# Kernel optimization log

Measured on AMD Instinct MI355X. Metric: run time of the kernel, lower is better.

Reference implementation:

```python
import jax, jax.numpy as jnp
import numpy as np

ALPHA = 0.2  # LeakyReLU negative slope
NEG_BIG = -9e15


def setup_inputs() -> dict:
    key = jax.random.key(0)
    k1, k2, k3, k4 = jax.random.split(key, 4)
    N, F_IN, F_OUT = 8192, 256, 128
    h = jax.random.normal(k1, (N, F_IN), dtype=jnp.float32)
    adj = jax.random.randint(k2, (N, N), 0, 2, dtype=jnp.int32)
    # xavier_uniform with gain=1.414
    def xavier(k, shape, gain=1.414):
        fan_in, fan_out = shape[0], shape[1]
        bound = gain * np.sqrt(6.0 / (fan_in + fan_out))
        return jax.random.uniform(k, shape, jnp.float32, -bound, bound)
    W = xavier(k3, (F_IN, F_OUT))
    a = xavier(k4, (2 * F_OUT, 1))
    return {"h": h, "adj": adj, "W": W, "a": a}


def reference(h, adj, W, a):
    # Wh: [N, F_out]
    Wh = h @ W
    F_out = W.shape[1]
    a1 = a[:F_out, 0]   # attends to source (row) node
    a2 = a[F_out:, 0]   # attends to target (col) node
    # Additive decomposition of concat([Wh_i, Wh_j]) @ a:
    # e[i, j] = leaky_relu(Wh_i . a1 + Wh_j . a2)
    f1 = Wh @ a1  # [N]
    f2 = Wh @ a2  # [N]
    e = jax.nn.leaky_relu(f1[:, None] + f2[None, :], negative_slope=ALPHA)  # [N, N]
    scores = jnp.where(adj > 0, e, jnp.float32(NEG_BIG))
    attention = jax.nn.softmax(scores, axis=1)
    # dropout is identity in eval mode (training=False)
    h_prime = attention @ Wh  # [N, F_out]
    return h_prime
```

## Files before the change

kernel.cpp:

```cpp
#include <hip/hip_runtime.h>


#define N_NODES 8192
#define F_IN 256
#define F_OUT 128
#define RPB 32
#define JCH 128
#define JSPLIT 4
#define JRANGE (N_NODES / JSPLIT)
#define NCH (JRANGE / JCH)

typedef _Float16 half8 __attribute__((ext_vector_type(8)));
typedef float floatx4 __attribute__((ext_vector_type(4)));
typedef float f32x4 __attribute__((ext_vector_type(4)));
typedef int intx4 __attribute__((ext_vector_type(4)));

__device__ __align__(16) float g_Wh[N_NODES * F_OUT];
__device__ __align__(16) _Float16 g_WhT[(size_t)F_OUT * N_NODES];
__device__ __align__(16) float g_f1[N_NODES];
__device__ __align__(16) float g_f2[N_NODES];
__device__ __align__(16) float g_part[JSPLIT][N_NODES * F_OUT];
__device__ __align__(16) float g_spart[JSPLIT][N_NODES];
__device__ __align__(16) unsigned char g_bits[(size_t)N_NODES * (N_NODES / 8)];

__global__ __launch_bounds__(256, 2) void prep_kernel(
    const int* __restrict__ adj, const float* __restrict__ h,
    const float* __restrict__ W, const float* __restrict__ a) {
  const int t = threadIdx.x;
  const int bid = blockIdx.x;

  if (bid < N_NODES / 8) {
    const int wave = t >> 6;
    const int lane = t & 63;
    const int row0 = bid * 8 + wave * 2;
#pragma unroll 1
    for (int rr = 0; rr < 2; ++rr) {
      const int r = row0 + rr;
      const int* rowp = adj + (size_t)r * N_NODES;
#pragma unroll 4
      for (int p = 0; p < 16; ++p) {
        const int j0 = p * 512 + lane * 8;
        const intx4 v0 = __builtin_nontemporal_load((const intx4*)(rowp + j0));
        const intx4 v1 = __builtin_nontemporal_load((const intx4*)(rowp + j0 + 4));
        unsigned int byte = 0;
        byte |= (v0.x != 0) ? 1u : 0u;
        byte |= (v0.y != 0) ? 2u : 0u;
        byte |= (v0.z != 0) ? 4u : 0u;
        byte |= (v0.w != 0) ? 8u : 0u;
        byte |= (v1.x != 0) ? 16u : 0u;
        byte |= (v1.y != 0) ? 32u : 0u;
        byte |= (v1.z != 0) ? 64u : 0u;
        byte |= (v1.w != 0) ? 128u : 0u;
        const int b = p * 64 + lane;
        const int addr = r * 1024 + (((b >> 2) & 3) * 4 + (b & 3)) * 64 + (b >> 4);
        g_bits[addr] = (unsigned char)byte;
      }
    }
    return;
  }

  __shared__ float hT[F_IN][20];
  __shared__ float fs[2][2][8][2];
  const int i0 = (bid - N_NODES / 8) * 16;
  {
    const int row = t >> 4;
    const int fu = t & 15;
#pragma unroll
    for (int r = 0; r < 4; ++r) {
      const int ku = r * 16 + fu;
      const f32x4 v = __builtin_nontemporal_load(
          (const f32x4*)(h + (size_t)(i0 + row) * F_IN + ku * 4));
      hT[ku * 4 + 0][row] = v.x; hT[ku * 4 + 1][row] = v.y;
      hT[ku * 4 + 2][row] = v.z; hT[ku * 4 + 3][row] = v.w;
    }
  }
  __syncthreads();
  const int c = t & 127;
  const int rg = t >> 7;
  float acc[8];
#pragma unroll
  for (int r = 0; r < 8; ++r) acc[r] = 0.f;
#pragma unroll 8
  for (int k = 0; k < F_IN; ++k) {
    const float wv = W[k * F_OUT + c];
    const float4 x0 = *(const float4*)(&hT[k][rg * 8]);
    const float4 x1 = *(const float4*)(&hT[k][rg * 8 + 4]);
    acc[0] = fmaf(x0.x, wv, acc[0]); acc[1] = fmaf(x0.y, wv, acc[1]);
    acc[2] = fmaf(x0.z, wv, acc[2]); acc[3] = fmaf(x0.w, wv, acc[3]);
    acc[4] = fmaf(x1.x, wv, acc[4]); acc[5] = fmaf(x1.y, wv, acc[5]);
    acc[6] = fmaf(x1.z, wv, acc[6]); acc[7] = fmaf(x1.w, wv, acc[7]);
  }
#pragma unroll
  for (int r = 0; r < 8; ++r)
    g_Wh[(size_t)(i0 + rg * 8 + r) * F_OUT + c] = acc[r];
  union { _Float16 hh[8]; uint4 u4; } pk;
#pragma unroll
  for (int r = 0; r < 8; ++r) pk.hh[r] = (_Float16)acc[r];
  *(uint4*)(g_WhT + (size_t)c * N_NODES + i0 + rg * 8) = pk.u4;

  const float a1c = a[c];
  const float a2c = a[F_OUT + c];
  float p1[8], p2[8];
#pragma unroll
  for (int r = 0; r < 8; ++r) { p1[r] = acc[r] * a1c; p2[r] = acc[r] * a2c; }
#pragma unroll
  for (int o = 32; o > 0; o >>= 1)
#pragma unroll
    for (int r = 0; r < 8; ++r) {
      p1[r] += __shfl_down(p1[r], o, 64);
      p2[r] += __shfl_down(p2[r], o, 64);
    }
  const int wv = t >> 6;
  const int lane = t & 63;
  if (lane == 0) {
#pragma unroll
    for (int r = 0; r < 8; ++r) {
      fs[wv >> 1][wv & 1][r][0] = p1[r];
      fs[wv >> 1][wv & 1][r][1] = p2[r];
    }
  }
  __syncthreads();
  if (t < 16) {
    const int rg2 = t >> 3, r2 = t & 7;
    g_f1[i0 + rg2 * 8 + r2] = fs[rg2][0][r2][0] + fs[rg2][1][r2][0];
    g_f2[i0 + rg2 * 8 + r2] = fs[rg2][0][r2][1] + fs[rg2][1][r2][1];
  }
}

__device__ __forceinline__ float score_b(unsigned int bit, float f2v, float f1r) {
  float s = f1r + f2v;
  s = fmaxf(s, 0.2f * s);
  float arg = bit ? fmaf(s, 1.44269504088896f, -16.0f) : -1.0e5f;
  return __builtin_amdgcn_exp2f(arg);
}

__global__ __launch_bounds__(256, 2) void gat_attn_kernel() {
  const int t = threadIdx.x;
  const int wave = t >> 6;
  const int lane = t & 63;
  const int mrow = lane & 15;
  const int quad = lane >> 4;
  const int flat = blockIdx.x;
  const int js = flat & 3;
  const int i0 = (flat >> 2) * RPB;
  const int jbase = js * JRANGE;

  __shared__ float ldsF2[JRANGE];
  __shared__ float ldsO[RPB][F_OUT];
  __shared__ float ldsS[4][RPB];

  int rm[4], cm[4];
  {
    half8 a1f, b1f, a2f, b2f;
#pragma unroll
    for (int e = 0; e < 8; ++e) {
      a1f[e] = (_Float16)0; b1f[e] = (_Float16)0;
      a2f[e] = (_Float16)0; b2f[e] = (_Float16)0;
    }
    if (quad == 0) {
      a1f[0] = (_Float16)mrow; b1f[0] = (_Float16)1;
      a2f[0] = (_Float16)1;    b2f[0] = (_Float16)mrow;
    }
    floatx4 d1 = (floatx4)0.f, d2 = (floatx4)0.f;
    d1 = __builtin_amdgcn_mfma_f32_16x16x32_f16(a1f, b1f, d1, 0, 0, 0);
    d2 = __builtin_amdgcn_mfma_f32_16x16x32_f16(a2f, b2f, d2, 0, 0, 0);
#pragma unroll
    for (int r = 0; r < 4; ++r) { rm[r] = (int)d1[r]; cm[r] = (int)d2[r]; }
  }

  const float f1r0 = g_f1[i0 + mrow];
  const float f1r1 = g_f1[i0 + 16 + mrow];

  half8 ones;
#pragma unroll
  for (int e = 0; e < 8; ++e) ones[e] = (_Float16)1;

  floatx4 acc[2][8];
  floatx4 asum[2];
#pragma unroll
  for (int tl = 0; tl < 2; ++tl) {
    asum[tl] = (floatx4)0.f;
#pragma unroll
    for (int ct = 0; ct < 8; ++ct) acc[tl][ct] = (floatx4)0.f;
  }

#pragma unroll
  for (int it = 0; it < 2; ++it) {
    const int u = it * 256 + t;
    *(float4*)&ldsF2[u * 4] = *(const float4*)(g_f2 + jbase + u * 4);
  }
  __syncthreads();

  const int wq = wave * 4 + quad;
  const int jloc = wave * 32 + quad * 8;
  const unsigned char* bp0 = g_bits + (i0 + mrow) * 1024 + wq * 64 + js * (JRANGE / 128);
  const unsigned char* bp1 = g_bits + (i0 + 16 + mrow) * 1024 + wq * 64 + js * (JRANGE / 128);

#pragma unroll 1
  for (int c4 = 0; c4 < NCH / 4; ++c4) {
    const unsigned int dw0 =
        __builtin_nontemporal_load((const unsigned int*)(bp0 + c4 * 4));
    const unsigned int dw1 =
        __builtin_nontemporal_load((const unsigned int*)(bp1 + c4 * 4));
#pragma unroll
    for (int k = 0; k < 4; ++k) {
      const int c = c4 * 4 + k;
      const int jglob = jbase + c * JCH + jloc;

      half8 bfr[8];
#pragma unroll
      for (int ct = 0; ct < 8; ++ct)
        bfr[ct] = *(const half8*)(g_WhT + (size_t)(ct * 16 + mrow) * N_NODES + jglob);

      const float4 F0 = *(const float4*)&ldsF2[c * JCH + jloc];
      const float4 F1 = *(const float4*)&ldsF2[c * JCH + jloc + 4];

      const unsigned int b0 = (dw0 >> (8 * k)) & 0xffu;
      const unsigned int b1 = (dw1 >> (8 * k)) & 0xffu;

      half8 af0, af1;
      af0[0] = (_Float16)score_b(b0 & 1u,   F0.x, f1r0);
      af0[1] = (_Float16)score_b(b0 & 2u,   F0.y, f1r0);
      af0[2] = (_Float16)score_b(b0 & 4u,   F0.z, f1r0);
      af0[3] = (_Float16)score_b(b0 & 8u,   F0.w, f1r0);
      af0[4] = (_Float16)score_b(b0 & 16u,  F1.x, f1r0);
      af0[5] = (_Float16)score_b(b0 & 32u,  F1.y, f1r0);
      af0[6] = (_Float16)score_b(b0 & 64u,  F1.z, f1r0);
      af0[7] = (_Float16)score_b(b0 & 128u, F1.w, f1r0);
      af1[0] = (_Float16)score_b(b1 & 1u,   F0.x, f1r1);
      af1[1] = (_Float16)score_b(b1 & 2u,   F0.y, f1r1);
      af1[2] = (_Float16)score_b(b1 & 4u,   F0.z, f1r1);
      af1[3] = (_Float16)score_b(b1 & 8u,   F0.w, f1r1);
      af1[4] = (_Float16)score_b(b1 & 16u,  F1.x, f1r1);
      af1[5] = (_Float16)score_b(b1 & 32u,  F1.y, f1r1);
      af1[6] = (_Float16)score_b(b1 & 64u,  F1.z, f1r1);
      af1[7] = (_Float16)score_b(b1 & 128u, F1.w, f1r1);

#pragma unroll
      for (int ct = 0; ct < 8; ++ct) {
        acc[0][ct] = __builtin_amdgcn_mfma_f32_16x16x32_f16(af0, bfr[ct], acc[0][ct], 0, 0, 0);
        acc[1][ct] = __builtin_amdgcn_mfma_f32_16x16x32_f16(af1, bfr[ct], acc[1][ct], 0, 0, 0);
      }
      asum[0] = __builtin_amdgcn_mfma_f32_16x16x32_f16(af0, ones, asum[0], 0, 0, 0);
      asum[1] = __builtin_amdgcn_mfma_f32_16x16x32_f16(af1, ones, asum[1], 0, 0, 0);
    }
  }

  if (mrow == 0) {
#pragma unroll
    for (int tl = 0; tl < 2; ++tl)
#pragma unroll
      for (int r = 0; r < 4; ++r)
        ldsS[wave][tl * 16 + rm[r]] = asum[tl][r];
  }
  for (int w = 0; w < 4; ++w) {
    if (wave == w) {
#pragma unroll
      for (int tl = 0; tl < 2; ++tl)
#pragma unroll
        for (int ct = 0; ct < 8; ++ct)
#pragma unroll
          for (int r = 0; r < 4; ++r) {
            float* p = &ldsO[tl * 16 + rm[r]][ct * 16 + cm[r]];
            if (w == 0) *p = acc[tl][ct][r];
            else        *p += acc[tl][ct][r];
          }
    }
    __syncthreads();
  }
  {
    const int row = t >> 3;
    const int c0 = (t & 7) * 16;
    float* dst = g_part[js] + (size_t)(i0 + row) * F_OUT + c0;
#pragma unroll
    for (int q = 0; q < 4; ++q)
      __builtin_nontemporal_store(*(const f32x4*)(&ldsO[row][c0 + q * 4]),
                                  (f32x4*)(dst + q * 4));
    if (t < RPB)
      g_spart[js][i0 + t] = ldsS[0][t] + ldsS[1][t] + ldsS[2][t] + ldsS[3][t];
  }
}

__global__ __launch_bounds__(256) void comb_kernel(float* __restrict__ out) {
  const int u = blockIdx.x * 256 + threadIdx.x;
  const int row = u >> 5;
  const float s = g_spart[0][row] + g_spart[1][row] +
                  g_spart[2][row] + g_spart[3][row];
  const f32x4 v = __builtin_nontemporal_load(((const f32x4*)g_part[0]) + u) +
                  __builtin_nontemporal_load(((const f32x4*)g_part[1]) + u) +
                  __builtin_nontemporal_load(((const f32x4*)g_part[2]) + u) +
                  __builtin_nontemporal_load(((const f32x4*)g_part[3]) + u);
  __builtin_nontemporal_store(v * (1.0f / s), ((f32x4*)out) + u);
}

extern "C" void kernel_launch(void* const* d_in, const int* in_sizes, int n_in,
                              void* d_out, int out_size, void* d_ws, size_t ws_size,
                              hipStream_t stream) {
  const float* h = (const float*)d_in[0];
  const int* adj = (const int*)d_in[1];
  const float* W = (const float*)d_in[2];
  const float* a = (const float*)d_in[3];
  float* out = (float*)d_out;
  (void)d_ws; (void)ws_size;

  prep_kernel<<<dim3(N_NODES / 8 + N_NODES / 16), dim3(256), 0, stream>>>(adj, h, W, a);
  gat_attn_kernel<<<dim3((N_NODES / RPB) * JSPLIT), dim3(256), 0, stream>>>();
  comb_kernel<<<dim3(N_NODES * F_OUT / 4 / 256), dim3(256), 0, stream>>>(out);
}
```

Measured before the change: 470.3 us.

## Stage WhT j-tiles in LDS and split attention over 32 column tiles

The attention kernel now gives each block a 256-column j-tile and 256 rows (8 waves). The fp16 WhT tile is staged once in padded shared memory, so the B operands are read from LDS instead of being re-gathered from global memory in every iteration. The adjacency bitmask is repacked so each lane reads its 8 bytes of mask in one load. The prep kernel interleaves bit-packing blocks with matmul blocks and no longer writes the unused fp32 Wh. In exchange, partial outputs grow from 4 to 32 slices, which adds a large amount of global write and read traffic in the combine kernel.

```diff
diff --git a/kernel.cpp b/kernel.cpp
--- a/kernel.cpp
+++ b/kernel.cpp
@@ -4,23 +4,21 @@
 #define N_NODES 8192
 #define F_IN 256
 #define F_OUT 128
-#define RPB 32
-#define JCH 128
-#define JSPLIT 4
-#define JRANGE (N_NODES / JSPLIT)
-#define NCH (JRANGE / JCH)
+#define NJT 32
+#define JTW 256
+#define NCH 8
+#define LDS_STRIDE 264
 
 typedef _Float16 half8 __attribute__((ext_vector_type(8)));
 typedef float floatx4 __attribute__((ext_vector_type(4)));
 typedef float f32x4 __attribute__((ext_vector_type(4)));
 typedef int intx4 __attribute__((ext_vector_type(4)));
 
-__device__ __align__(16) float g_Wh[N_NODES * F_OUT];
 __device__ __align__(16) _Float16 g_WhT[(size_t)F_OUT * N_NODES];
 __device__ __align__(16) float g_f1[N_NODES];
 __device__ __align__(16) float g_f2[N_NODES];
-__device__ __align__(16) float g_part[JSPLIT][N_NODES * F_OUT];
-__device__ __align__(16) float g_spart[JSPLIT][N_NODES];
+__device__ __align__(16) float g_part[NJT][N_NODES * F_OUT];
+__device__ __align__(16) float g_spart[NJT][N_NODES];
 __device__ __align__(16) unsigned char g_bits[(size_t)N_NODES * (N_NODES / 8)];
 
 __global__ __launch_bounds__(256, 2) void prep_kernel(
@@ -29,10 +27,11 @@
   const int t = threadIdx.x;
   const int bid = blockIdx.x;
 
-  if (bid < N_NODES / 8) {
+  if (bid % 3 != 0) {
+    const int pid = bid - (bid + 2) / 3;
     const int wave = t >> 6;
     const int lane = t & 63;
-    const int row0 = bid * 8 + wave * 2;
+    const int row0 = pid * 8 + wave * 2;
 #pragma unroll 1
     for (int rr = 0; rr < 2; ++rr) {
       const int r = row0 + rr;
@@ -52,8 +51,7 @@
         byte |= (v1.z != 0) ? 64u : 0u;
         byte |= (v1.w != 0) ? 128u : 0u;
         const int b = p * 64 + lane;
-        const int addr = r * 1024 + (((b >> 2) & 3) * 4 + (b & 3)) * 64 + (b >> 4);
-        g_bits[addr] = (unsigned char)byte;
+        g_bits[(size_t)r * 1024 + (b & 3) * 256 + (b >> 2)] = (unsigned char)byte;
       }
     }
     return;
@@ -61,7 +59,7 @@
 
   __shared__ float hT[F_IN][20];
   __shared__ float fs[2][2][8][2];
-  const int i0 = (bid - N_NODES / 8) * 16;
+  const int i0 = (bid / 3) * 16;
   {
     const int row = t >> 4;
     const int fu = t & 15;
@@ -90,9 +88,6 @@
     acc[4] = fmaf(x1.x, wv, acc[4]); acc[5] = fmaf(x1.y, wv, acc[5]);
     acc[6] = fmaf(x1.z, wv, acc[6]); acc[7] = fmaf(x1.w, wv, acc[7]);
   }
-#pragma unroll
-  for (int r = 0; r < 8; ++r)
-    g_Wh[(size_t)(i0 + rg * 8 + r) * F_OUT + c] = acc[r];
   union { _Float16 hh[8]; uint4 u4; } pk;
 #pragma unroll
   for (int r = 0; r < 8; ++r) pk.hh[r] = (_Float16)acc[r];
@@ -134,20 +129,25 @@
   return __builtin_amdgcn_exp2f(arg);
 }
 
-__global__ __launch_bounds__(256, 2) void gat_attn_kernel() {
+__global__ __launch_bounds__(512, 2) void gat_attn_kernel() {
   const int t = threadIdx.x;
   const int wave = t >> 6;
   const int lane = t & 63;
   const int mrow = lane & 15;
   const int quad = lane >> 4;
-  const int flat = blockIdx.x;
-  const int js = flat & 3;
-  const int i0 = (flat >> 2) * RPB;
-  const int jbase = js * JRANGE;
-
-  __shared__ float ldsF2[JRANGE];
-  __shared__ float ldsO[RPB][F_OUT];
-  __shared__ float ldsS[4][RPB];
+  const int bid = blockIdx.x;
+  const int jt = bid >> 5;
+  const int ig = bid & 31;
+  const int rowb = ig * 256 + wave * 32;
+
+  __shared__ _Float16 ldsWhT[F_OUT * LDS_STRIDE];
+  __shared__ float ldsF2[JTW];
+
+  const int r0 = rowb + mrow, r1 = rowb + 16 + mrow;
+  const uint2 AB0 = *(const uint2*)(g_bits + (size_t)r0 * 1024 + quad * 256 + jt * 8);
+  const uint2 AB1 = *(const uint2*)(g_bits + (size_t)r1 * 1024 + quad * 256 + jt * 8);
+  const float f1r0 = g_f1[r0];
+  const float f1r1 = g_f1[r1];
 
   int rm[4], cm[4];
   {
@@ -168,8 +168,15 @@
     for (int r = 0; r < 4; ++r) { rm[r] = (int)d1[r]; cm[r] = (int)d2[r]; }
   }
 
-  const float f1r0 = g_f1[i0 + mrow];
-  const float f1r1 = g_f1[i0 + 16 + mrow];
+#pragma unroll
+  for (int it = 0; it < 8; ++it) {
+    const int idx = it * 512 + t;
+    const int row = idx >> 5, cu = idx & 31;
+    *(half8*)&ldsWhT[row * LDS_STRIDE + cu * 8] =
+        *(const half8*)(g_WhT + (size_t)row * N_NODES + jt * JTW + cu * 8);
+  }
+  if (t < 64) *(float4*)&ldsF2[t * 4] = *(const float4*)(g_f2 + jt * JTW + t * 4);
+  __syncthreads();
 
   half8 ones;
 #pragma unroll
@@ -185,111 +192,75 @@
   }
 
 #pragma unroll
-  for (int it = 0; it < 2; ++it) {
-    const int u = it * 256 + t;
-    *(float4*)&ldsF2[u * 4] = *(const float4*)(g_f2 + jbase + u * 4);
-  }
-  __syncthreads();
-
-  const int wq = wave * 4 + quad;
-  const int jloc = wave * 32 + quad * 8;
-  const unsigned char* bp0 = g_bits + (i0 + mrow) * 1024 + wq * 64 + js * (JRANGE / 128);
-  const unsigned char* bp1 = g_bits + (i0 + 16 + mrow) * 1024 + wq * 64 + js * (JRANGE / 128);
-
-#pragma unroll 1
-  for (int c4 = 0; c4 < NCH / 4; ++c4) {
-    const unsigned int dw0 =
-        __builtin_nontemporal_load((const unsigned int*)(bp0 + c4 * 4));
-    const unsigned int dw1 =
-        __builtin_nontemporal_load((const unsigned int*)(bp1 + c4 * 4));
-#pragma unroll
-    for (int k = 0; k < 4; ++k) {
-      const int c = c4 * 4 + k;
-      const int jglob = jbase + c * JCH + jloc;
-
-      half8 bfr[8];
-#pragma unroll
-      for (int ct = 0; ct < 8; ++ct)
-        bfr[ct] = *(const half8*)(g_WhT + (size_t)(ct * 16 + mrow) * N_NODES + jglob);
-
-      const float4 F0 = *(const float4*)&ldsF2[c * JCH + jloc];
-      const float4 F1 = *(const float4*)&ldsF2[c * JCH + jloc + 4];
-
-      const unsigned int b0 = (dw0 >> (8 * k)) & 0xffu;
-      const unsigned int b1 = (dw1 >> (8 * k)) & 0xffu;
-
-      half8 af0, af1;
-      af0[0] = (_Float16)score_b(b0 & 1u,   F0.x, f1r0);
-      af0[1] = (_Float16)score_b(b0 & 2u,   F0.y, f1r0);
-      af0[2] = (_Float16)score_b(b0 & 4u,   F0.z, f1r0);
-      af0[3] = (_Float16)score_b(b0 & 8u,   F0.w, f1r0);
-      af0[4] = (_Float16)score_b(b0 & 16u,  F1.x, f1r0);
-      af0[5] = (_Float16)score_b(b0 & 32u,  F1.y, f1r0);
-      af0[6] = (_Float16)score_b(b0 & 64u,  F1.z, f1r0);
-      af0[7] = (_Float16)score_b(b0 & 128u, F1.w, f1r0);
-      af1[0] = (_Float16)score_b(b1 & 1u,   F0.x, f1r1);
-      af1[1] = (_Float16)score_b(b1 & 2u,   F0.y, f1r1);
-      af1[2] = (_Float16)score_b(b1 & 4u,   F0.z, f1r1);
-      af1[3] = (_Float16)score_b(b1 & 8u,   F0.w, f1r1);
-      af1[4] = (_Float16)score_b(b1 & 16u,  F1.x, f1r1);
-      af1[5] = (_Float16)score_b(b1 & 32u,  F1.y, f1r1);
-      af1[6] = (_Float16)score_b(b1 & 64u,  F1.z, f1r1);
-      af1[7] = (_Float16)score_b(b1 & 128u, F1.w, f1r1);
-
-#pragma unroll
-      for (int ct = 0; ct < 8; ++ct) {
-        acc[0][ct] = __builtin_amdgcn_mfma_f32_16x16x32_f16(af0, bfr[ct], acc[0][ct], 0, 0, 0);
-        acc[1][ct] = __builtin_amdgcn_mfma_f32_16x16x32_f16(af1, bfr[ct], acc[1][ct], 0, 0, 0);
-      }
-      asum[0] = __builtin_amdgcn_mfma_f32_16x16x32_f16(af0, ones, asum[0], 0, 0, 0);
-      asum[1] = __builtin_amdgcn_mfma_f32_16x16x32_f16(af1, ones, asum[1], 0, 0, 0);
-    }
-  }
-
+  for (int ch = 0; ch < NCH; ++ch) {
+    const int kb = ch * 32 + quad * 8;
+
+    half8 bfr[8];
+#pragma unroll
+    for (int ct = 0; ct < 8; ++ct)
+      bfr[ct] = *(const half8*)&ldsWhT[(ct * 16 + mrow) * LDS_STRIDE + kb];
+
+    const float4 F0 = *(const float4*)&ldsF2[kb];
+    const float4 F1 = *(const float4*)&ldsF2[kb + 4];
+
+    const unsigned int b0 = ((ch & 4) ? AB0.y : AB0.x) >> ((ch & 3) * 8);
+    const unsigned int b1 = ((ch & 4) ? AB1.y : AB1.x) >> ((ch & 3) * 8);
+
+    half8 af0, af1;
+    af0[0] = (_Float16)score_b(b0 & 1u,   F0.x, f1r0);
+    af0[1] = (_Float16)score_b(b0 & 2u,   F0.y, f1r0);
+    af0[2] = (_Float16)score_b(b0 & 4u,   F0.z, f1r0);
+    af0[3] = (_Float16)score_b(b0 & 8u,   F0.w, f1r0);
+    af0[4] = (_Float16)score_b(b0 & 16u,  F1.x, f1r0);
+    af0[5] = (_Float16)score_b(b0 & 32u,  F1.y, f1r0);
+    af0[6] = (_Float16)score_b(b0 & 64u,  F1.z, f1r0);
+    af0[7] = (_Float16)score_b(b0 & 128u, F1.w, f1r0);
+    af1[0] = (_Float16)score_b(b1 & 1u,   F0.x, f1r1);
+    af1[1] = (_Float16)score_b(b1 & 2u,   F0.y, f1r1);
+    af1[2] = (_Float16)score_b(b1 & 4u,   F0.z, f1r1);
+    af1[3] = (_Float16)score_b(b1 & 8u,   F0.w, f1r1);
+    af1[4] = (_Float16)score_b(b1 & 16u,  F1.x, f1r1);
+    af1[5] = (_Float16)score_b(b1 & 32u,  F1.y, f1r1);
+    af1[6] = (_Float16)score_b(b1 & 64u,  F1.z, f1r1);
+    af1[7] = (_Float16)score_b(b1 & 128u, F1.w, f1r1);
+
+#pragma unroll
+    for (int ct = 0; ct < 8; ++ct) {
+      acc[0][ct] = __builtin_amdgcn_mfma_f32_16x16x32_f16(af0, bfr[ct], acc[0][ct], 0, 0, 0);
+      acc[1][ct] = __builtin_amdgcn_mfma_f32_16x16x32_f16(af1, bfr[ct], acc[1][ct], 0, 0, 0);
+    }
+    asum[0] = __builtin_amdgcn_mfma_f32_16x16x32_f16(af0, ones, asum[0], 0, 0, 0);
+    asum[1] = __builtin_amdgcn_mfma_f32_16x16x32_f16(af1, ones, asum[1], 0, 0, 0);
+  }
+
+  float* pslice = g_part[jt];
+#pragma unroll
+  for (int tl = 0; tl < 2; ++tl)
+#pragma unroll
+    for (int ct = 0; ct < 8; ++ct)
+#pragma unroll
+      for (int r = 0; r < 4; ++r)
+        pslice[(size_t)(rowb + tl * 16 + rm[r]) * F_OUT + ct * 16 + cm[r]] =
+            acc[tl][ct][r];
   if (mrow == 0) {
 #pragma unroll
     for (int tl = 0; tl < 2; ++tl)
 #pragma unroll
       for (int r = 0; r < 4; ++r)
-        ldsS[wave][tl * 16 + rm[r]] = asum[tl][r];
-  }
-  for (int w = 0; w < 4; ++w) {
-    if (wave == w) {
-#pragma unroll
-      for (int tl = 0; tl < 2; ++tl)
-#pragma unroll
-        for (int ct = 0; ct < 8; ++ct)
-#pragma unroll
-          for (int r = 0; r < 4; ++r) {
-            float* p = &ldsO[tl * 16 + rm[r]][ct * 16 + cm[r]];
-            if (w == 0) *p = acc[tl][ct][r];
-            else        *p += acc[tl][ct][r];
-          }
-    }
-    __syncthreads();
-  }
-  {
-    const int row = t >> 3;
-    const int c0 = (t & 7) * 16;
-    float* dst = g_part[js] + (size_t)(i0 + row) * F_OUT + c0;
-#pragma unroll
-    for (int q = 0; q < 4; ++q)
-      __builtin_nontemporal_store(*(const f32x4*)(&ldsO[row][c0 + q * 4]),
-                                  (f32x4*)(dst + q * 4));
-    if (t < RPB)
-      g_spart[js][i0 + t] = ldsS[0][t] + ldsS[1][t] + ldsS[2][t] + ldsS[3][t];
+        g_spart[jt][rowb + tl * 16 + rm[r]] = asum[tl][r];
   }
 }
 
 __global__ __launch_bounds__(256) void comb_kernel(float* __restrict__ out) {
   const int u = blockIdx.x * 256 + threadIdx.x;
   const int row = u >> 5;
-  const float s = g_spart[0][row] + g_spart[1][row] +
-                  g_spart[2][row] + g_spart[3][row];
-  const f32x4 v = __builtin_nontemporal_load(((const f32x4*)g_part[0]) + u) +
-                  __builtin_nontemporal_load(((const f32x4*)g_part[1]) + u) +
-                  __builtin_nontemporal_load(((const f32x4*)g_part[2]) + u) +
-                  __builtin_nontemporal_load(((const f32x4*)g_part[3]) + u);
+  float s = 0.f;
+  f32x4 v = (f32x4)0.f;
+#pragma unroll
+  for (int q = 0; q < NJT; ++q) {
+    s += g_spart[q][row];
+    v += *(((const f32x4*)g_part[q]) + u);
+  }
   __builtin_nontemporal_store(v * (1.0f / s), ((f32x4*)out) + u);
 }
 
@@ -303,7 +274,7 @@
   float* out = (float*)d_out;
   (void)d_ws; (void)ws_size;
 
-  prep_kernel<<<dim3(N_NODES / 8 + N_NODES / 16), dim3(256), 0, stream>>>(adj, h, W, a);
-  gat_attn_kernel<<<dim3((N_NODES / RPB) * JSPLIT), dim3(256), 0, stream>>>();
+  prep_kernel<<<dim3(1536), dim3(256), 0, stream>>>(adj, h, W, a);
+  gat_attn_kernel<<<dim3(NJT * 32), dim3(512), 0, stream>>>();
   comb_kernel<<<dim3(N_NODES * F_OUT / 4 / 256), dim3(256), 0, stream>>>(out);
 }
```

Result: faster. 432.0 us (-8.1%).
